# Kernel tuning notes

Hardware: AMD Instinct MI355X
Metric: run time of the kernel (lower is better)

Reference implementation:

```python
import math
import jax, jax.numpy as jnp
import numpy as np
from jax import lax

PI = math.pi

def _gauss1d(ks, sigma):
    # kornia gaussian: centered at (ks-1)/2 for both odd and even ks
    x = jnp.arange(ks, dtype=jnp.float32) - (ks - 1) / 2.0
    g = jnp.exp(-0.5 * (x / sigma) ** 2)
    return g / g.sum()

def _unfold_nonoverlap(x, k):
    # F.unfold(x, kernel_size=k, stride=k) for x (B,1,H,W), H,W divisible by k
    B, C, H, W = x.shape
    nH, nW = H // k, W // k
    p = x.reshape(B, nH, k, nW, k).transpose(0, 2, 4, 1, 3)
    return p.reshape(B, k * k, nH * nW)

def _sift(x, ps, nab=8, nsb=4, clipval=0.2, eps=1e-10):
    # kornia SIFTDescriptor(patch_size=ps), x: (N,1,ps,ps) -> (N,128)
    N = x.shape[0]
    g1 = _gauss1d(ps, ps / math.sqrt(2.0))
    gk = jnp.outer(g1, g1)  # (ps,ps), sum 1
    # spatial_gradient mode='diff', normalized, replicate pad
    xp = jnp.pad(x, ((0, 0), (0, 0), (0, 0), (1, 1)), mode='edge')
    gx = 0.5 * (xp[..., 2:] - xp[..., :-2])
    yp = jnp.pad(x, ((0, 0), (0, 0), (1, 1), (0, 0)), mode='edge')
    gy = 0.5 * (yp[:, :, 2:, :] - yp[:, :, :-2, :])
    mag = jnp.sqrt(gx * gx + gy * gy + eps) * gk  # (N,1,ps,ps)
    ori = jnp.arctan2(gy, gx + eps) + 2.0 * PI
    o_big = nab * ori / (2.0 * PI)
    bo0f = jnp.floor(o_big)
    w1 = o_big - bo0f
    bo0 = bo0f.astype(jnp.int32) % nab
    bo1 = (bo0 + 1) % nab
    c0 = jax.nn.one_hot(bo0[:, 0], nab, axis=1, dtype=x.dtype)  # (N,8,ps,ps)
    c1 = jax.nn.one_hot(bo1[:, 0], nab, axis=1, dtype=x.dtype)
    bins = c0 * ((1.0 - w1) * mag) + c1 * (w1 * mag)  # (N,8,ps,ps)
    # triangular pooling kernel, depthwise conv over the 8 angular bins
    bk = 2 * (ps // (nsb + 1)); stride = ps // nsb; pad = bk // 4
    half = bk / 2.0
    xc2 = half - jnp.abs(jnp.arange(bk, dtype=jnp.float32) + 0.5 - half)
    pk = jnp.outer(xc2, xc2) / (half * half)
    pk = jnp.tile(pk[None, None], (nab, 1, 1, 1))  # (8,1,bk,bk)
    pooled = lax.conv_general_dilated(bins, pk, (stride, stride),
        [(pad, pad), (pad, pad)], feature_group_count=nab,
        dimension_numbers=('NCHW', 'OIHW', 'NCHW'))  # (N,8,4,4)
    d = pooled.reshape(N, -1)
    d = d / jnp.maximum(jnp.linalg.norm(d, axis=1, keepdims=True), 1e-12)
    d = jnp.clip(d, 0.0, clipval)
    d = d / jnp.maximum(jnp.linalg.norm(d, axis=1, keepdims=True), 1e-12)
    d = jnp.sqrt(d / jnp.maximum(jnp.abs(d).sum(1, keepdims=True), 1e-12) + eps)  # rootsift
    return d

def _conv_t(x, w, b, stride=2, pad=1):
    # torch ConvTranspose2d; w: (Cin,Cout,k,k)
    k = w.shape[-1]
    wT = jnp.transpose(jnp.flip(w, (-2, -1)), (1, 0, 2, 3))  # (Cout,Cin,k,k)
    y = lax.conv_general_dilated(x, wT, (1, 1),
        [(k - 1 - pad, k - 1 - pad)] * 2, lhs_dilation=(stride, stride),
        dimension_numbers=('NCHW', 'OIHW', 'NCHW'))
    return y + b[None, :, None, None]

def _gn(x, groups, w, b, eps=1e-5):
    N, C, H, W = x.shape
    xg = x.reshape(N, groups, -1)
    mean = xg.mean(-1, keepdims=True)
    var = ((xg - mean) ** 2).mean(-1, keepdims=True)
    xn = ((xg - mean) * lax.rsqrt(var + eps)).reshape(N, C, H, W)
    return xn * w[None, :, None, None] + b[None, :, None, None]

def _jbf(x, guide, ky, kx, sigma_color, sy, sx):
    # kornia joint_bilateral_blur, border='reflect', color_distance='l1'
    B, C, H, W = x.shape
    py, px = ky // 2, kx // 2
    xp = jnp.pad(x, ((0, 0), (0, 0), (py, py), (px, px)), mode='reflect')
    gp = jnp.pad(guide, ((0, 0), (0, 0), (py, py), (px, px)), mode='reflect')
    def win(p):
        return jnp.stack([p[:, :, i:i + H, j:j + W] for i in range(ky) for j in range(kx)], axis=-1)
    ux, ug = win(xp), win(gp)  # (B,C,H,W,ky*kx)
    diff = ug - guide[..., None]
    cd2 = jnp.square(jnp.sum(jnp.abs(diff), axis=1, keepdims=True))
    ck = jnp.exp((-0.5 / (sigma_color ** 2)) * cd2)  # (B,1,H,W,K)
    sk = jnp.outer(_gauss1d(ky, sy), _gauss1d(kx, sx)).reshape(1, 1, 1, 1, -1)
    kern = sk * ck
    return (ux * kern).sum(-1) / kern.sum(-1)

def _forward(x, d1w, d1b, g1w, g1b, s1w, s1b, d2w, d2b, g2w, g2b, s2w, s2b,
             d3w, d3b, g3w, g3b, d4w, d4b, g4w, g4b, fw, fb):
    B = x.shape[0]
    s7 = _sift(_unfold_nonoverlap(x, 7).reshape(-1, 1, 32, 32), 32).reshape(B, 128, 7, 7)
    h = jax.nn.relu(_gn(_conv_t(s7, d1w, d1b), 8, g1w, g1b))  # (B,32,14,14); dropout=identity (eval)
    s14 = _sift(_unfold_nonoverlap(x, 14).reshape(-1, 1, 16, 16), 16).reshape(B, 128, 14, 14)
    sk1 = jnp.einsum('bchw,oc->bohw', s14, s1w[:, :, 0, 0]) + s1b[None, :, None, None]
    h = jax.nn.relu(_gn(_conv_t(jnp.concatenate([h, sk1], 1), d2w, d2b), 4, g2w, g2b))  # (B,16,28,28)
    s28 = _sift(_unfold_nonoverlap(x, 28).reshape(-1, 1, 8, 8), 8).reshape(B, 128, 28, 28)
    sk2 = jnp.einsum('bchw,oc->bohw', s28, s2w[:, :, 0, 0]) + s2b[None, :, None, None]
    h = jax.nn.relu(_gn(_conv_t(jnp.concatenate([h, sk2], 1), d3w, d3b), 2, g3w, g3b))  # (B,8,56,56)
    h = jax.nn.relu(_gn(_conv_t(h, d4w, d4b), 1, g4w, g4b))  # (B,4,112,112)
    h = _conv_t(h, fw, fb)  # (B,2,224,224)
    h = _jbf(h, jnp.tile(x, (1, 2, 1, 1)), 5, 5, 0.1, 1.5, 1.5)
    scale = jnp.array([0.436, 0.615], dtype=h.dtype)
    return jnp.tanh(h) * scale[None, :, None, None]

def setup_inputs() -> dict:
    key = jax.random.key(0)
    ks = jax.random.split(key, 8)
    B = 16
    f32 = jnp.float32
    def rn(k, shp, s=0.05):
        return jax.random.normal(k, shp, f32) * s
    return {
        'x': jax.random.uniform(ks[0], (B, 1, 224, 224), f32),
        'd1w': rn(ks[1], (128, 32, 4, 4)), 'd1b': jnp.zeros((32,), f32),
        'g1w': jnp.ones((32,), f32), 'g1b': jnp.zeros((32,), f32),
        's1w': rn(ks[2], (32, 128, 1, 1)), 's1b': jnp.zeros((32,), f32),
        'd2w': rn(ks[3], (64, 16, 4, 4)), 'd2b': jnp.zeros((16,), f32),
        'g2w': jnp.ones((16,), f32), 'g2b': jnp.zeros((16,), f32),
        's2w': rn(ks[4], (16, 128, 1, 1)), 's2b': jnp.zeros((16,), f32),
        'd3w': rn(ks[5], (32, 8, 4, 4)), 'd3b': jnp.zeros((8,), f32),
        'g3w': jnp.ones((8,), f32), 'g3b': jnp.zeros((8,), f32),
        'd4w': rn(ks[6], (8, 4, 4, 4)), 'd4b': jnp.zeros((4,), f32),
        'g4w': jnp.ones((4,), f32), 'g4b': jnp.zeros((4,), f32),
        'fw': rn(ks[7], (4, 2, 4, 4)), 'fb': jnp.zeros((2,), f32),
    }

def reference(x, d1w, d1b, g1w, g1b, s1w, s1b, d2w, d2b, g2w, g2b, s2w, s2b,
              d3w, d3b, g3w, g3b, d4w, d4b, g4w, g4b, fw, fb):
    return _forward(x, d1w, d1b, g1w, g1b, s1w, s1b, d2w, d2b, g2w, g2b, s2w, s2b,
                    d3w, d3b, g3w, g3b, d4w, d4b, g4w, g4b, fw, fb)
```

## Files before the change

### kernel.cpp

```cpp
#include <hip/hip_runtime.h>
#include <math.h>

#define PI_F 3.14159265358979323846f

template<int PS, int K>
__device__ __forceinline__
void sift_block(const float* __restrict__ x, float* __restrict__ out,
                int n, float* lds)
{
    constexpr int NT = 256;
    constexpr int NPIX = PS*PS;
    constexpr int NPIXP = NPIX + 1;
    constexpr int BK = 2*(PS/5);
    constexpr int STRIDE = PS/4;
    constexpr int PAD = BK/4;
    constexpr float HALF = BK*0.5f;
    constexpr int NWAVE = NT/64;
    constexpr int ROWS = BK/2;

    float* patch = lds;
    float* bins  = patch + NPIX;
    float* g1    = bins + 8*NPIXP;
    float* pool2 = g1 + PS;
    float* wred  = pool2 + 128;
    float* gsum_s = wred + NWAVE;

    const int tid = threadIdx.x;
    const int b = n / (K*K);
    const int c = n % (K*K);
    const int ki = c / K;
    const int kj = c % K;

    const float* xb = x + (size_t)b*224*224;
    for (int idx = tid; idx < NPIX; idx += NT) {
        int i = idx / PS, j = idx - i*PS;
        patch[idx] = xb[(i*K + ki)*224 + (j*K + kj)];
    }
    if (tid < PS) {
        const float sigma = (float)PS * 0.70710678118654752440f;
        float xv = (float)tid - (PS-1)*0.5f;
        float t = xv / sigma;
        g1[tid] = expf(-0.5f*t*t);
    }
    for (int idx = tid; idx < 8*NPIXP; idx += NT) bins[idx] = 0.f;
    __syncthreads();
    if (tid == 0) {
        float s = 0.f;
        for (int i = 0; i < PS; i++) s += g1[i];
        gsum_s[0] = s;
    }
    __syncthreads();
    const float ginv = 1.0f / (gsum_s[0]*gsum_s[0]);

    for (int idx = tid; idx < NPIX; idx += NT) {
        int i = idx / PS, j = idx - i*PS;
        int jm = j > 0 ? j-1 : 0, jp = j < PS-1 ? j+1 : PS-1;
        int im = i > 0 ? i-1 : 0, ip = i < PS-1 ? i+1 : PS-1;
        float gx = 0.5f*(patch[i*PS+jp] - patch[i*PS+jm]);
        float gy = 0.5f*(patch[ip*PS+j] - patch[im*PS+j]);
        float mag = sqrtf(gx*gx + gy*gy + 1e-10f) * (g1[i]*g1[j]*ginv);
        float ori = atan2f(gy, gx + 1e-10f) + 2.f*PI_F;
        float obig = ori * (8.f/(2.f*PI_F));
        float bo0f = floorf(obig);
        float w1 = obig - bo0f;
        int bo0 = ((int)bo0f) & 7;
        int bo1 = (bo0 + 1) & 7;
        bins[bo0*NPIXP + idx] = (1.f - w1)*mag;
        bins[bo1*NPIXP + idx] = w1*mag;
    }
    __syncthreads();

    float pacc = 0.f;
    const int t = tid & 127;
    const int half = tid >> 7;
    {
        int o = t >> 4;
        int py = (t >> 2) & 3;
        int px = t & 3;
        int sy = py*STRIDE - PAD;
        int sx = px*STRIDE - PAD;
        const float* bo = bins + o*NPIXP;
        for (int dr = 0; dr < ROWS; dr++) {
            int di = half*ROWS + dr;
            int i = sy + di;
            if (i < 0 || i >= PS) continue;
            float wi = HALF - fabsf((float)di + 0.5f - HALF);
            for (int dj = 0; dj < BK; dj++) {
                int j = sx + dj;
                if (j < 0 || j >= PS) continue;
                float wj = HALF - fabsf((float)dj + 0.5f - HALF);
                pacc += bo[i*PS + j] * (wi*wj);
            }
        }
    }
    if (half == 1) pool2[t] = pacc;
    __syncthreads();
    float d = 0.f;
    if (tid < 128) {
        d = (pacc + pool2[tid]) * (1.0f/(HALF*HALF));
    }

    const int wv = tid >> 6;
    const int ln = tid & 63;

    float v = d*d;
    #pragma unroll
    for (int off = 32; off > 0; off >>= 1) v += __shfl_down(v, off);
    if (ln == 0) wred[wv] = v;
    __syncthreads();
    float nrm = 0.f;
    #pragma unroll
    for (int w2 = 0; w2 < NWAVE; w2++) nrm += wred[w2];
    nrm = sqrtf(nrm);
    __syncthreads();
    d = d / fmaxf(nrm, 1e-12f);
    d = fminf(fmaxf(d, 0.f), 0.2f);

    v = d*d;
    #pragma unroll
    for (int off = 32; off > 0; off >>= 1) v += __shfl_down(v, off);
    if (ln == 0) wred[wv] = v;
    __syncthreads();
    nrm = 0.f;
    #pragma unroll
    for (int w2 = 0; w2 < NWAVE; w2++) nrm += wred[w2];
    nrm = sqrtf(nrm);
    __syncthreads();
    d = d / fmaxf(nrm, 1e-12f);

    v = d;
    #pragma unroll
    for (int off = 32; off > 0; off >>= 1) v += __shfl_down(v, off);
    if (ln == 0) wred[wv] = v;
    __syncthreads();
    float ssum = 0.f;
    #pragma unroll
    for (int w2 = 0; w2 < NWAVE; w2++) ssum += wred[w2];
    d = sqrtf(d / fmaxf(ssum, 1e-12f) + 1e-10f);

    if (tid < 128) out[(size_t)n*128 + tid] = d;
}

__device__ __forceinline__
void sift8_block(const float* __restrict__ x, float* __restrict__ out, int bid)
{
    const int tid = threadIdx.x;
    const int l = tid & 63;
    const int wv = tid >> 6;
    const int n = bid*4 + wv;
    const int b = n / 784;
    const int c = n % 784;
    const int ki = c / 28, kj = c % 28;
    const int i = l >> 3, j = l & 7;

    const float* xb = x + (size_t)b*50176;
    float v = xb[(i*28 + ki)*224 + (j*28 + kj)];

    int lL = (j > 0) ? l-1 : l;
    int lR = (j < 7) ? l+1 : l;
    int lU = (i > 0) ? l-8 : l;
    int lD = (i < 7) ? l+8 : l;
    float pL = __shfl(v, lL);
    float pR = __shfl(v, lR);
    float pU = __shfl(v, lU);
    float pD = __shfl(v, lD);
    float gx = 0.5f*(pR - pL);
    float gy = 0.5f*(pD - pU);

    float ti = ((float)i - 3.5f) * (1.f/5.65685424949238f);
    float tj = ((float)j - 3.5f) * (1.f/5.65685424949238f);
    float wsp = __expf(-0.5f*(ti*ti + tj*tj));
    float mag = sqrtf(gx*gx + gy*gy + 1e-10f) * wsp;
    float ori = atan2f(gy, gx + 1e-10f) + 2.f*PI_F;
    float obig = ori * (8.f/(2.f*PI_F));
    float bo0f = floorf(obig);
    float w1 = obig - bo0f;
    int bo0 = ((int)bo0f) & 7;
    int bo1 = (bo0 + 1) & 7;
    float c0 = (1.f - w1)*mag;
    float c1 = w1*mag;

    const int t = ((i & 1) << 1) | (j & 1);
    float d0 = 0.f, d1 = 0.f;
    #pragma unroll
    for (int o = 0; o < 8; o++) {
        float val = (bo0 == o ? c0 : 0.f) + (bo1 == o ? c1 : 0.f);
        val += __shfl_xor(val, 1);
        val += __shfl_xor(val, 8);
        if (o == 2*t)     d0 = val;
        if (o == 2*t + 1) d1 = val;
    }

    float s = d0*d0 + d1*d1;
    #pragma unroll
    for (int off = 32; off > 0; off >>= 1) s += __shfl_xor(s, off);
    float nrm = fmaxf(sqrtf(s), 1e-12f);
    d0 /= nrm; d1 /= nrm;
    d0 = fminf(fmaxf(d0, 0.f), 0.2f);
    d1 = fminf(fmaxf(d1, 0.f), 0.2f);
    s = d0*d0 + d1*d1;
    #pragma unroll
    for (int off = 32; off > 0; off >>= 1) s += __shfl_xor(s, off);
    nrm = fmaxf(sqrtf(s), 1e-12f);
    d0 /= nrm; d1 /= nrm;
    s = d0 + d1;
    #pragma unroll
    for (int off = 32; off > 0; off >>= 1) s += __shfl_xor(s, off);
    s = fmaxf(s, 1e-12f);
    d0 = sqrtf(d0/s + 1e-10f);
    d1 = sqrtf(d1/s + 1e-10f);

    int cell = (i >> 1)*4 + (j >> 1);
    float* ob = out + (size_t)n*128 + cell;
    ob[(2*t)*16]     = d0;
    ob[(2*t + 1)*16] = d1;
}

__global__ __launch_bounds__(256)
void sift_all(const float* __restrict__ x, float* __restrict__ s7,
              float* __restrict__ s14, float* __restrict__ s28)
{
    __shared__ float lds[9408];
    const int bid = blockIdx.x;
    if (bid < 784) {
        sift_block<32, 7>(x, s7, bid, lds);
    } else if (bid < 3920) {
        sift_block<16, 14>(x, s14, bid - 784, lds);
    } else {
        sift8_block(x, s28, bid - 3920);
    }
}

template<int CO, int S>
__device__ __forceinline__
void conv1x1_block(const float* __restrict__ in, const float* __restrict__ w,
                   const float* __restrict__ bias, float* __restrict__ out,
                   int bid, float* wt)
{
    const int tid = threadIdx.x;
    for (int i = tid; i < 128*CO; i += 256) {
        int c = i / CO, co = i - c*CO;
        wt[i] = w[co*128 + c];
    }
    __syncthreads();
    int idx = bid*256 + tid;
    int s = idx % S; int r = idx / S;
    int co4 = r % (CO/4); int b = r / (CO/4);
    int co = co4*4;
    const float* ib = in + (size_t)b*128*S + s;
    float acc0 = bias[co], acc1 = bias[co+1], acc2 = bias[co+2], acc3 = bias[co+3];
    #pragma unroll 8
    for (int c = 0; c < 128; c++) {
        float v = ib[c*S];
        const float4 wv = *(const float4*)&wt[c*CO + co];
        acc0 += v*wv.x; acc1 += v*wv.y; acc2 += v*wv.z; acc3 += v*wv.w;
    }
    float* ob = out + ((size_t)b*CO + co)*S + s;
    ob[0] = acc0; ob[S] = acc1; ob[2*S] = acc2; ob[3*S] = acc3;
}

__device__ __forceinline__
void convt_l1_block(const float* __restrict__ in0, const float* __restrict__ w,
                    const float* __restrict__ bias,
                    float* __restrict__ out, float2* __restrict__ pst_out,
                    int by, float* lds)
{
    constexpr int CIN = 128, COUT = 32, HIN = 7, NCH = 4, NT = 256;
    constexpr int H0 = 14, SP = 196, HIN2 = 49;
    constexpr int NR = 9, WIN = 9, TILE = CIN*NR*WIN;
    constexpr int WSTRIDE = CIN*NCH*4 + 4;

    float* tile  = lds;
    float* wl2   = tile + TILE;
    float* wpart = wl2 + 4*WSTRIDE;

    const int tid = threadIdx.x;
    const int b  = by >> 3;
    const int cb = by & 7;
    const int c0 = cb*NCH;

    for (int idx = tid; idx < 4*CIN*NCH*4; idx += NT) {
        int k = idx & 3;
        int t2 = idx >> 2;
        int j = t2 % NCH; t2 /= NCH;
        int ci = t2 % CIN;
        int pq = t2 / CIN;
        int pA = pq >> 1, qA = pq & 1;
        int dy = pA + 2*(k>>1), dx = qA + 2*(k&1);
        wl2[pq*WSTRIDE + (ci*NCH + j)*4 + k] = w[(ci*COUT + c0 + j)*16 + dy*4 + dx];
    }
    const float* i0 = in0 + (size_t)b*CIN*HIN2;
    for (int idx = tid; idx < TILE; idx += NT) {
        int c = idx % WIN;
        int t2 = idx / WIN;
        int r = t2 % NR;
        int ci = t2 / NR;
        int iy = r - 1, ix = c - 1;
        float v = 0.f;
        if (iy >= 0 && iy < HIN && ix >= 0 && ix < HIN)
            v = i0[ci*HIN2 + iy*HIN + ix];
        tile[idx] = v;
    }
    __syncthreads();

    float acc[NCH];
    #pragma unroll
    for (int j = 0; j < NCH; j++) acc[j] = 0.f;

    const bool active = tid < SP;
    if (active) {
        int oy = tid / H0, ox = tid % H0;
        int pA = (oy+1)&1, qA = (ox+1)&1;
        int iyA = (oy+1-pA)>>1, ixA = (ox+1-qA)>>1;
        int toff = (iyA+1)*WIN + (ixA+1);
        const float* wbase = wl2 + (pA*2+qA)*WSTRIDE;

        #pragma unroll
        for (int j = 0; j < NCH; j++) acc[j] = bias[c0 + j];

        #pragma unroll 4
        for (int ci = 0; ci < CIN; ci++) {
            const float* tp = tile + ci*(NR*WIN) + toff;
            float l0 = tp[0];
            float l1 = tp[-1];
            float l2 = tp[-WIN];
            float l3 = tp[-WIN-1];
            const float* wr = wbase + ci*NCH*4;
            #pragma unroll
            for (int j = 0; j < NCH; j++) {
                const float4 wv = *(const float4*)(wr + j*4);
                acc[j] += l0*wv.x + l1*wv.y + l2*wv.z + l3*wv.w;
            }
        }
        float* ob = out + ((size_t)b*COUT + c0)*SP + tid;
        #pragma unroll
        for (int j = 0; j < NCH; j++) ob[j*SP] = acc[j];
    }

    const int wv = tid >> 6;
    const int ln = tid & 63;
    float ps = 0.f, pq2 = 0.f;
    #pragma unroll
    for (int j = 0; j < NCH; j++) {
        float v = active ? acc[j] : 0.f;
        ps += v; pq2 += v*v;
    }
    #pragma unroll
    for (int off = 32; off > 0; off >>= 1) {
        ps  += __shfl_down(ps,  off);
        pq2 += __shfl_down(pq2, off);
    }
    if (ln == 0) { wpart[wv*2] = ps; wpart[wv*2+1] = pq2; }
    __syncthreads();
    if (tid == 0) {
        float s0 = wpart[0]+wpart[2]+wpart[4]+wpart[6];
        float s1 = wpart[1]+wpart[3]+wpart[5]+wpart[7];
        pst_out[(size_t)b*8 + cb] = make_float2(s0, s1);
    }
}

__global__ __launch_bounds__(256)
void skip_l1(const float* __restrict__ s14, const float* __restrict__ s28,
             const float* __restrict__ s1w, const float* __restrict__ s1b,
             const float* __restrict__ s2w, const float* __restrict__ s2b,
             const float* __restrict__ s7,  const float* __restrict__ d1w,
             const float* __restrict__ d1b,
             float* __restrict__ sk1, float* __restrict__ sk2,
             float* __restrict__ h1, float2* __restrict__ pst1)
{
    __shared__ float lds[18584];
    const int bid = blockIdx.x;
    if (bid < 98)       conv1x1_block<32, 196>(s14, s1w, s1b, sk1, bid, lds);
    else if (bid < 294) conv1x1_block<16, 784>(s28, s2w, s2b, sk2, bid - 98, lds);
    else                convt_l1_block(s7, d1w, d1b, h1, pst1, bid - 294, lds);
}

template<int CIN0, int CIN1, int COUT, int G, int HIN, int NCH, int RT, int NT,
         bool FUSE, int GIN, int NGIN, int NBLK_IN, int NBLK_OUT>
__global__ __launch_bounds__(NT)
void convt_tiled(const float* __restrict__ in0, const float* __restrict__ in1,
                 const float* __restrict__ w, const float* __restrict__ bias,
                 const float2* __restrict__ pst_in,
                 const float* __restrict__ gnw, const float* __restrict__ gnb,
                 float* __restrict__ out, float2* __restrict__ pst_out)
{
    constexpr int CIN = CIN0 + CIN1;
    constexpr int CG = COUT / G;
    constexpr int NGRP = NCH / CG;
    constexpr int CB = COUT / NCH;
    constexpr int H0 = 2*HIN;
    constexpr int SP = H0*H0;
    constexpr int HIN2 = HIN*HIN;
    constexpr int NR = RT/2 + 2;
    constexpr int WIN = HIN + 2;
    constexpr int TILE = CIN*NR*WIN;
    constexpr int WSTRIDE = CIN*NCH*4 + 4;
    constexpr int NPOS = RT*H0;
    constexpr int NWAVE = NT/64;

    __shared__ float tile[TILE];
    __shared__ float wl2[4*WSTRIDE];
    __shared__ float a_s[CIN0];
    __shared__ float b_s[CIN0];
    __shared__ float wpart[NWAVE][NGRP][2];

    const int tid = threadIdx.x;
    const int by = blockIdx.y;
    const int bx = blockIdx.x;
    const int b  = by / CB;
    const int cb = by - b*CB;
    const int c0 = cb*NCH;
    const int g0 = c0 / CG;
    const int r0 = bx * RT;
    const int row0 = r0/2 - 1;

    if constexpr (FUSE) {
        if (tid < CIN0) {
            int gi = tid / (CIN0/GIN);
            float s0 = 0.f, s1 = 0.f;
            for (int k = 0; k < NBLK_IN; k++) {
                float2 p = pst_in[((size_t)b*GIN + gi)*NBLK_IN + k];
                s0 += p.x; s1 += p.y;
            }
            float mean = s0 * (1.f/NGIN);
            float var  = s1 * (1.f/NGIN) - mean*mean;
            float inv  = rsqrtf(var + 1e-5f);
            float a = inv * gnw[tid];
            a_s[tid] = a;
            b_s[tid] = gnb[tid] - mean*a;
        }
        __syncthreads();
    }

    for (int idx = tid; idx < 4*CIN*NCH*4; idx += NT) {
        int k = idx & 3;
        int t2 = idx >> 2;
        int j = t2 % NCH; t2 /= NCH;
        int ci = t2 % CIN;
        int pq = t2 / CIN;
        int pA = pq >> 1, qA = pq & 1;
        int dy = pA + 2*(k>>1), dx = qA + 2*(k&1);
        wl2[pq*WSTRIDE + (ci*NCH + j)*4 + k] = w[(ci*COUT + c0 + j)*16 + dy*4 + dx];
    }

    const float* i0 = in0 + (size_t)b*CIN0*HIN2;
    for (int idx = tid; idx < TILE; idx += NT) {
        int c = idx % WIN;
        int t2 = idx / WIN;
        int r = t2 % NR;
        int ci = t2 / NR;
        int iy = row0 + r, ix = c - 1;
        float v = 0.f;
        if (iy >= 0 && iy < HIN && ix >= 0 && ix < HIN) {
            if (CIN1 == 0 || ci < CIN0) {
                v = i0[ci*HIN2 + iy*HIN + ix];
                if constexpr (FUSE) v = fmaxf(v*a_s[ci] + b_s[ci], 0.f);
            } else {
                v = in1[((size_t)b*CIN1 + (ci-CIN0))*HIN2 + iy*HIN + ix];
            }
        }
        tile[idx] = v;
    }
    __syncthreads();

    float acc[NCH];
    #pragma unroll
    for (int j = 0; j < NCH; j++) acc[j] = 0.f;

    const bool active = tid < NPOS;
    if (active) {
        int oy = r0 + tid / H0, ox = tid % H0;
        int pA = (oy+1)&1, qA = (ox+1)&1;
        int iyA = (oy+1-pA)>>1, ixA = (ox+1-qA)>>1;
        int rA = iyA - row0;
        int cA = ixA + 1;
        int toff = rA*WIN + cA;
        const float* wbase = wl2 + (pA*2+qA)*WSTRIDE;

        #pragma unroll
        for (int j = 0; j < NCH; j++) acc[j] = bias[c0 + j];

        #pragma unroll 4
        for (int ci = 0; ci < CIN; ci++) {
            const float* tp = tile + ci*(NR*WIN) + toff;
            float l0 = tp[0];
            float l1 = tp[-1];
            float l2 = tp[-WIN];
            float l3 = tp[-WIN-1];
            const float* wr = wbase + ci*NCH*4;
            #pragma unroll
            for (int j = 0; j < NCH; j++) {
                const float4 wv = *(const float4*)(wr + j*4);
                acc[j] += l0*wv.x + l1*wv.y + l2*wv.z + l3*wv.w;
            }
        }
        float* ob = out + ((size_t)b*COUT + c0)*SP + r0*H0 + tid;
        #pragma unroll
        for (int j = 0; j < NCH; j++) ob[j*SP] = acc[j];
    }

    const int wv = tid >> 6;
    const int ln = tid & 63;
    #pragma unroll
    for (int grp = 0; grp < NGRP; grp++) {
        float ps = 0.f, pq2 = 0.f;
        #pragma unroll
        for (int j = 0; j < CG; j++) {
            float v = active ? acc[grp*CG + j] : 0.f;
            ps += v; pq2 += v*v;
        }
        #pragma unroll
        for (int off = 32; off > 0; off >>= 1) {
            ps  += __shfl_down(ps,  off);
            pq2 += __shfl_down(pq2, off);
        }
        if (ln == 0) { wpart[wv][grp][0] = ps; wpart[wv][grp][1] = pq2; }
    }
    __syncthreads();
    if (tid < NGRP) {
        float s0 = 0.f, s1 = 0.f;
        #pragma unroll
        for (int w2 = 0; w2 < NWAVE; w2++) { s0 += wpart[w2][tid][0]; s1 += wpart[w2][tid][1]; }
        pst_out[((size_t)b*G + g0 + tid)*NBLK_OUT + bx] = make_float2(s0, s1);
    }
}

__global__ __launch_bounds__(256)
void final_bilateral(const float* __restrict__ h4, const float* __restrict__ fw,
                     const float* __restrict__ fb, const float2* __restrict__ pst_in,
                     const float* __restrict__ gnw, const float* __restrict__ gnb,
                     const float* __restrict__ x, float* __restrict__ out)
{
    const float g[5] = {0.1200783f, 0.2338817f, 0.2920800f, 0.2338817f, 0.1200783f};
    __shared__ float xs[400], p0s[400], p1s[400];
    __shared__ float wl2[128];
    __shared__ float a_s[4], b_s[4], bl[2], mv[2];

    const int tid = threadIdx.x;
    const int b = blockIdx.z;
    const int ty0 = blockIdx.y*16;
    const int tx0 = blockIdx.x*16;
    const float* xb = x + (size_t)b*50176;

    if (tid < 128) {
        int k = tid & 3;
        int t = tid >> 2;
        int co = t & 1; t >>= 1;
        int ci = t & 3;
        int pq = t >> 2;
        int pA = pq >> 1, qA = pq & 1;
        int dy = pA + 2*(k>>1), dx = qA + 2*(k&1);
        wl2[tid] = fw[(ci*2 + co)*16 + dy*4 + dx];
    }
    if (tid < 2) bl[tid] = fb[tid];
    if (tid >= 192) {
        int k0 = tid - 192;
        float s0 = 0.f, s1 = 0.f;
        if (k0 < 56) {
            float2 p = pst_in[(size_t)b*56 + k0];
            s0 = p.x; s1 = p.y;
        }
        #pragma unroll
        for (int off = 32; off > 0; off >>= 1) {
            s0 += __shfl_down(s0, off);
            s1 += __shfl_down(s1, off);
        }
        if (k0 == 0) {
            float mean = s0 * (1.f/50176.f);
            float var  = s1 * (1.f/50176.f) - mean*mean;
            mv[0] = mean;
            mv[1] = rsqrtf(var + 1e-5f);
        }
    }
    __syncthreads();
    if (tid < 4) {
        float a = mv[1] * gnw[tid];
        a_s[tid] = a;
        b_s[tid] = gnb[tid] - mv[0]*a;
    }
    __syncthreads();

    const float* ib = h4 + (size_t)b*4*12544;
    for (int idx = tid; idx < 400; idx += 256) {
        int r = idx / 20, cc = idx - r*20;
        int oy = ty0 - 2 + r;  oy = oy < 0 ? -oy : (oy > 223 ? 446 - oy : oy);
        int ox = tx0 - 2 + cc; ox = ox < 0 ? -ox : (ox > 223 ? 446 - ox : ox);
        xs[idx] = xb[oy*224 + ox];

        int pA = (oy+1)&1, iyA = (oy+1-pA)>>1, iyB = iyA-1;
        int qA = (ox+1)&1, ixA = (ox+1-qA)>>1, ixB = ixA-1;
        float mYA = (iyA < 112) ? 1.f : 0.f;
        float mYB = (iyB >= 0)  ? 1.f : 0.f;
        float mXA = (ixA < 112) ? 1.f : 0.f;
        float mXB = (ixB >= 0)  ? 1.f : 0.f;
        float m0 = mYA*mXA, m1 = mYA*mXB, m2 = mYB*mXA, m3 = mYB*mXB;
        int iyAc = min(iyA, 111), iyBc = max(iyB, 0);
        int ixAc = min(ixA, 111), ixBc = max(ixB, 0);
        int oAA = iyAc*112 + ixAc, oAB = iyAc*112 + ixBc;
        int oBA = iyBc*112 + ixAc, oBB = iyBc*112 + ixBc;
        const float* wbase = wl2 + (pA*2+qA)*32;

        float acc0 = bl[0], acc1 = bl[1];
        #pragma unroll
        for (int ci = 0; ci < 4; ci++) {
            const float* ip = ib + ci*12544;
            float a = a_s[ci], bb = b_s[ci];
            float l0 = fmaxf(ip[oAA]*a + bb, 0.f);
            float l1 = fmaxf(ip[oAB]*a + bb, 0.f);
            float l2 = fmaxf(ip[oBA]*a + bb, 0.f);
            float l3 = fmaxf(ip[oBB]*a + bb, 0.f);
            float t0 = l0*m0, t1 = l1*m1, t2 = l2*m2, t3 = l3*m3;
            const float4 w0 = *(const float4*)(wbase + ci*8);
            const float4 w1 = *(const float4*)(wbase + ci*8 + 4);
            acc0 += t0*w0.x + t1*w0.y + t2*w0.z + t3*w0.w;
            acc1 += t0*w1.x + t1*w1.y + t2*w1.z + t3*w1.w;
        }
        p0s[idx] = acc0;
        p1s[idx] = acc1;
    }
    __syncthreads();

    int ly = tid >> 4, lx = tid & 15;
    int base = (ly+2)*20 + (lx+2);
    float center = xs[base];
    float wsum = 0.f, a0 = 0.f, a1 = 0.f;
    #pragma unroll
    for (int di = -2; di <= 2; di++){
        #pragma unroll
        for (int dj = -2; dj <= 2; dj++){
            int o = base + di*20 + dj;
            float dg = xs[o] - center;
            float wgt = g[di+2]*g[dj+2]*__expf(-200.f*dg*dg);
            wsum += wgt;
            a0 += wgt * p0s[o];
            a1 += wgt * p1s[o];
        }
    }
    float inv = 1.0f / wsum;
    int s = (ty0 + ly)*224 + (tx0 + lx);
    out[(size_t)(b*2)*50176 + s]     = tanhf(a0*inv)*0.436f;
    out[(size_t)(b*2+1)*50176 + s]   = tanhf(a1*inv)*0.615f;
}

extern "C" void kernel_launch(void* const* d_in, const int* in_sizes, int n_in,
                              void* d_out, int out_size, void* d_ws, size_t ws_size,
                              hipStream_t stream) {
    (void)in_sizes; (void)n_in; (void)out_size; (void)ws_size;
    const float* x   = (const float*)d_in[0];
    const float* d1w = (const float*)d_in[1];
    const float* d1b = (const float*)d_in[2];
    const float* g1w = (const float*)d_in[3];
    const float* g1b = (const float*)d_in[4];
    const float* s1w = (const float*)d_in[5];
    const float* s1b = (const float*)d_in[6];
    const float* d2w = (const float*)d_in[7];
    const float* d2b = (const float*)d_in[8];
    const float* g2w = (const float*)d_in[9];
    const float* g2b = (const float*)d_in[10];
    const float* s2w = (const float*)d_in[11];
    const float* s2b = (const float*)d_in[12];
    const float* d3w = (const float*)d_in[13];
    const float* d3b = (const float*)d_in[14];
    const float* g3w = (const float*)d_in[15];
    const float* g3b = (const float*)d_in[16];
    const float* d4w = (const float*)d_in[17];
    const float* d4b = (const float*)d_in[18];
    const float* g4w = (const float*)d_in[19];
    const float* g4b = (const float*)d_in[20];
    const float* fw  = (const float*)d_in[21];
    const float* fb  = (const float*)d_in[22];
    float* out = (float*)d_out;

    float* ws  = (float*)d_ws;
    float* s7  = ws;
    float* s14 = s7  + 100352;
    float* s28 = s14 + 401408;
    float* sk1 = s28 + 1605632;
    float* sk2 = sk1 + 100352;
    float* h1  = sk2 + 200704;
    float* h2  = h1  + 100352;
    float* h3  = h2  + 200704;
    float* h4  = h3  + 401408;
    float2* pst1 = (float2*)(h4 + 802816);
    float2* pst2 = pst1 + 128;
    float2* pst3 = pst2 + 448;
    float2* pst4 = pst3 + 448;

    sift_all<<<7056, 256, 0, stream>>>(x, s7, s14, s28);

    skip_l1<<<422, 256, 0, stream>>>(s14, s28, s1w, s1b, s2w, s2b,
                                     s7, d1w, d1b, sk1, sk2, h1, pst1);

    convt_tiled< 32,32, 16, 4, 14, 8,  4, 128, true, 8, 784, 1, 7>
        <<<dim3(7, 16*2), 128, 0, stream>>>(h1, sk1, d2w, d2b, pst1, g1w, g1b, h2, pst2);
    convt_tiled< 16,16,  8, 2, 28, 8,  4, 256, true, 4, 3136, 7, 14>
        <<<dim3(14, 16), 256, 0, stream>>>(h2, sk2, d3w, d3b, pst2, g2w, g2b, h3, pst3);
    convt_tiled<  8, 0,  4, 1, 56, 4,  2, 256, true, 2, 12544, 14, 56>
        <<<dim3(56, 16), 256, 0, stream>>>(h3, nullptr, d4w, d4b, pst3, g3w, g3b, h4, pst4);

    final_bilateral<<<dim3(14, 14, 16), 256, 0, stream>>>(h4, fw, fb, pst4, g4w, g4b, x, out);
}
```

Measured before the change: 234.1 us.

## Store magnitude and orientation instead of 8 dense bins; single-wave normalization

Replaces the eight zero-initialized angular bin planes in LDS with two per-pixel arrays, magnitude and scaled orientation. Each pooling thread now recomputes the bin-split contribution for its own orientation on the fly. The Gaussian spatial weight is computed inline with a fast exp, removing the table, its serial sum and two barriers. The final three-pass descriptor normalization is done by a single wave using xor shuffles instead of block-wide reductions. LDS per block drops from about 37KB to 13KB, which should allow higher occupancy, at the cost of redundant floor and compare work in the pooling loop and slightly different rounding in the Gaussian weight.

```diff
diff --git a/kernel.cpp b/kernel.cpp
--- a/kernel.cpp
+++ b/kernel.cpp
@@ -10,20 +10,16 @@
 {
     constexpr int NT = 256;
     constexpr int NPIX = PS*PS;
-    constexpr int NPIXP = NPIX + 1;
     constexpr int BK = 2*(PS/5);
     constexpr int STRIDE = PS/4;
     constexpr int PAD = BK/4;
     constexpr float HALF = BK*0.5f;
-    constexpr int NWAVE = NT/64;
     constexpr int ROWS = BK/2;
 
     float* patch = lds;
-    float* bins  = patch + NPIX;
-    float* g1    = bins + 8*NPIXP;
-    float* pool2 = g1 + PS;
-    float* wred  = pool2 + 128;
-    float* gsum_s = wred + NWAVE;
+    float* magp  = patch + NPIX;
+    float* obp   = magp + NPIX;
+    float* pool2 = obp + NPIX;
 
     const int tid = threadIdx.x;
     const int b = n / (K*K);
@@ -36,50 +32,34 @@
         int i = idx / PS, j = idx - i*PS;
         patch[idx] = xb[(i*K + ki)*224 + (j*K + kj)];
     }
-    if (tid < PS) {
-        const float sigma = (float)PS * 0.70710678118654752440f;
-        float xv = (float)tid - (PS-1)*0.5f;
-        float t = xv / sigma;
-        g1[tid] = expf(-0.5f*t*t);
-    }
-    for (int idx = tid; idx < 8*NPIXP; idx += NT) bins[idx] = 0.f;
-    __syncthreads();
-    if (tid == 0) {
-        float s = 0.f;
-        for (int i = 0; i < PS; i++) s += g1[i];
-        gsum_s[0] = s;
-    }
-    __syncthreads();
-    const float ginv = 1.0f / (gsum_s[0]*gsum_s[0]);
-
+    __syncthreads();
+
+    const float inv_sig = 1.0f / ((float)PS * 0.70710678118654752440f);
     for (int idx = tid; idx < NPIX; idx += NT) {
         int i = idx / PS, j = idx - i*PS;
         int jm = j > 0 ? j-1 : 0, jp = j < PS-1 ? j+1 : PS-1;
         int im = i > 0 ? i-1 : 0, ip = i < PS-1 ? i+1 : PS-1;
         float gx = 0.5f*(patch[i*PS+jp] - patch[i*PS+jm]);
         float gy = 0.5f*(patch[ip*PS+j] - patch[im*PS+j]);
-        float mag = sqrtf(gx*gx + gy*gy + 1e-10f) * (g1[i]*g1[j]*ginv);
+        float ti = ((float)i - (PS-1)*0.5f) * inv_sig;
+        float tj = ((float)j - (PS-1)*0.5f) * inv_sig;
+        float wsp = __expf(-0.5f*(ti*ti + tj*tj));
+        float mag = sqrtf(gx*gx + gy*gy + 1e-10f) * wsp;
         float ori = atan2f(gy, gx + 1e-10f) + 2.f*PI_F;
-        float obig = ori * (8.f/(2.f*PI_F));
-        float bo0f = floorf(obig);
-        float w1 = obig - bo0f;
-        int bo0 = ((int)bo0f) & 7;
-        int bo1 = (bo0 + 1) & 7;
-        bins[bo0*NPIXP + idx] = (1.f - w1)*mag;
-        bins[bo1*NPIXP + idx] = w1*mag;
+        magp[idx] = mag;
+        obp[idx]  = ori * (8.f/(2.f*PI_F));
     }
     __syncthreads();
 
     float pacc = 0.f;
-    const int t = tid & 127;
-    const int half = tid >> 7;
     {
-        int o = t >> 4;
-        int py = (t >> 2) & 3;
-        int px = t & 3;
-        int sy = py*STRIDE - PAD;
-        int sx = px*STRIDE - PAD;
-        const float* bo = bins + o*NPIXP;
+        const int t = tid & 127;
+        const int half = tid >> 7;
+        const int o = t >> 4;
+        const int py = (t >> 2) & 3;
+        const int px = t & 3;
+        const int sy = py*STRIDE - PAD;
+        const int sx = px*STRIDE - PAD;
         for (int dr = 0; dr < ROWS; dr++) {
             int di = half*ROWS + dr;
             int i = sy + di;
@@ -89,56 +69,46 @@
                 int j = sx + dj;
                 if (j < 0 || j >= PS) continue;
                 float wj = HALF - fabsf((float)dj + 0.5f - HALF);
-                pacc += bo[i*PS + j] * (wi*wj);
+                float m  = magp[i*PS + j];
+                float ob = obp[i*PS + j];
+                float bo0f = floorf(ob);
+                float w1 = ob - bo0f;
+                int bo0 = ((int)bo0f) & 7;
+                int bo1 = (bo0 + 1) & 7;
+                float ctr = (bo0 == o ? (1.f - w1) : 0.f) + (bo1 == o ? w1 : 0.f);
+                pacc += ctr * m * (wi*wj);
             }
         }
     }
-    if (half == 1) pool2[t] = pacc;
-    __syncthreads();
-    float d = 0.f;
-    if (tid < 128) {
-        d = (pacc + pool2[tid]) * (1.0f/(HALF*HALF));
-    }
-
-    const int wv = tid >> 6;
-    const int ln = tid & 63;
-
-    float v = d*d;
-    #pragma unroll
-    for (int off = 32; off > 0; off >>= 1) v += __shfl_down(v, off);
-    if (ln == 0) wred[wv] = v;
-    __syncthreads();
-    float nrm = 0.f;
-    #pragma unroll
-    for (int w2 = 0; w2 < NWAVE; w2++) nrm += wred[w2];
-    nrm = sqrtf(nrm);
-    __syncthreads();
-    d = d / fmaxf(nrm, 1e-12f);
-    d = fminf(fmaxf(d, 0.f), 0.2f);
-
-    v = d*d;
-    #pragma unroll
-    for (int off = 32; off > 0; off >>= 1) v += __shfl_down(v, off);
-    if (ln == 0) wred[wv] = v;
-    __syncthreads();
-    nrm = 0.f;
-    #pragma unroll
-    for (int w2 = 0; w2 < NWAVE; w2++) nrm += wred[w2];
-    nrm = sqrtf(nrm);
-    __syncthreads();
-    d = d / fmaxf(nrm, 1e-12f);
-
-    v = d;
-    #pragma unroll
-    for (int off = 32; off > 0; off >>= 1) v += __shfl_down(v, off);
-    if (ln == 0) wred[wv] = v;
-    __syncthreads();
-    float ssum = 0.f;
-    #pragma unroll
-    for (int w2 = 0; w2 < NWAVE; w2++) ssum += wred[w2];
-    d = sqrtf(d / fmaxf(ssum, 1e-12f) + 1e-10f);
-
-    if (tid < 128) out[(size_t)n*128 + tid] = d;
+    pool2[tid] = pacc;
+    __syncthreads();
+
+    if (tid < 64) {
+        float d0 = pool2[tid]      + pool2[tid + 128];
+        float d1 = pool2[tid + 64] + pool2[tid + 192];
+
+        float s = d0*d0 + d1*d1;
+        #pragma unroll
+        for (int off = 32; off > 0; off >>= 1) s += __shfl_xor(s, off);
+        float nrm = fmaxf(sqrtf(s), 1e-12f);
+        d0 /= nrm; d1 /= nrm;
+        d0 = fminf(fmaxf(d0, 0.f), 0.2f);
+        d1 = fminf(fmaxf(d1, 0.f), 0.2f);
+        s = d0*d0 + d1*d1;
+        #pragma unroll
+        for (int off = 32; off > 0; off >>= 1) s += __shfl_xor(s, off);
+        nrm = fmaxf(sqrtf(s), 1e-12f);
+        d0 /= nrm; d1 /= nrm;
+        s = d0 + d1;
+        #pragma unroll
+        for (int off = 32; off > 0; off >>= 1) s += __shfl_xor(s, off);
+        s = fmaxf(s, 1e-12f);
+        d0 = sqrtf(d0/s + 1e-10f);
+        d1 = sqrtf(d1/s + 1e-10f);
+
+        out[(size_t)n*128 + tid]      = d0;
+        out[(size_t)n*128 + 64 + tid] = d1;
+    }
 }
 
 __device__ __forceinline__
@@ -220,7 +190,7 @@
 void sift_all(const float* __restrict__ x, float* __restrict__ s7,
               float* __restrict__ s14, float* __restrict__ s28)
 {
-    __shared__ float lds[9408];
+    __shared__ float lds[3328];
     const int bid = blockIdx.x;
     if (bid < 784) {
         sift_block<32, 7>(x, s7, bid, lds);
```

Result: faster. 226.2 us (-3.4%).
